# Performance work log

Measured on AMD Instinct MI355X. Metric: run time of the kernel, lower is better.

## Reference

```python
import jax, jax.numpy as jnp
import numpy as np

N_NODES = 10000
N_EDGES = 160000
BATCH = 16
F_IN = 32          # NODE_EMBED_SIZE
HEADS = 4
HDIM = 4
HC = HEADS * HDIM  # 16
N_LAYERS = 4
OBS_DIM = 100
NUM_OUT = 30
HID = 128
POOL_OUT = 15


def setup_inputs() -> dict:
    key = jax.random.key(0)
    ks = jax.random.split(key, 26)
    s = 0.1
    d = {}
    d["x"] = jax.random.normal(ks[0], (BATCH, N_NODES, F_IN), jnp.float32)
    d["obs"] = jax.random.normal(ks[1], (BATCH, OBS_DIM), jnp.float32)
    d["src"] = jax.random.randint(ks[2], (N_EDGES,), 0, N_NODES)
    d["dst"] = jax.random.randint(ks[3], (N_EDGES,), 0, N_NODES)
    # layer 0 (in=F_IN), layers 1..3 (in=HC) GATv2 params
    d["W0l"] = jax.random.normal(ks[4], (F_IN, HC)) * s
    d["W0r"] = jax.random.normal(ks[5], (F_IN, HC)) * s
    d["b0l"] = jnp.zeros((HC,), jnp.float32)
    d["b0r"] = jnp.zeros((HC,), jnp.float32)
    d["Wl"] = jax.random.normal(ks[6], (N_LAYERS - 1, HC, HC)) * s
    d["Wr"] = jax.random.normal(ks[7], (N_LAYERS - 1, HC, HC)) * s
    d["bl"] = jnp.zeros((N_LAYERS - 1, HC), jnp.float32)
    d["br"] = jnp.zeros((N_LAYERS - 1, HC), jnp.float32)
    d["att"] = jax.random.normal(ks[8], (N_LAYERS, HEADS, HDIM)) * s
    d["bias"] = jnp.zeros((N_LAYERS, HC), jnp.float32)
    # mean-pool aggregator projection to 15
    d["Wp"] = jax.random.normal(ks[9], (HC, POOL_OUT)) * s
    d["bp"] = jnp.zeros((POOL_OUT,), jnp.float32)
    # hybrid policy head: cat([feat15, obs100]) -> 128 -> 128 -> num_outputs
    d["W1"] = jax.random.normal(ks[10], (POOL_OUT + OBS_DIM, HID)) * s
    d["b1"] = jnp.zeros((HID,), jnp.float32)
    d["W2"] = jax.random.normal(ks[11], (HID, HID)) * s
    d["b2"] = jnp.zeros((HID,), jnp.float32)
    d["W3"] = jax.random.normal(ks[12], (HID, NUM_OUT)) * s
    d["b3"] = jnp.zeros((NUM_OUT,), jnp.float32)
    return d


def _gatv2_layer(x, src, dst, Wl, Wr, bl, br, att, bias):
    # x: [B,N,F]; src/dst: [E'] (self loops included); att: [H,C]
    B, N, _ = x.shape
    H, C = att.shape
    xl = (x @ Wl + bl).reshape(B, N, H, C)  # source transform
    xr = (x @ Wr + br).reshape(B, N, H, C)  # target transform
    z = jax.nn.leaky_relu(xl[:, src] + xr[:, dst], negative_slope=0.2)  # [B,E,H,C]
    e = jnp.einsum('behc,hc->ebh', z, att)  # [E,B,H] edge-major for segment ops
    m = jax.lax.stop_gradient(jax.ops.segment_max(e, dst, num_segments=N))
    m = jnp.where(jnp.isfinite(m), m, 0.0)
    ex = jnp.exp(e - m[dst])
    ssum = jax.ops.segment_sum(ex, dst, num_segments=N)
    alpha = ex / (ssum[dst] + 1e-16)  # softmax over incoming edges of dst
    msg = xl[:, src] * jnp.transpose(alpha, (1, 0, 2))[..., None]  # [B,E,H,C]
    out = jax.ops.segment_sum(jnp.transpose(msg, (1, 0, 2, 3)), dst, num_segments=N)
    return jnp.transpose(out, (1, 0, 2, 3)).reshape(B, N, H * C) + bias


def reference(x, obs, src, dst, W0l, W0r, b0l, b0r, Wl, Wr, bl, br, att, bias,
              Wp, bp, W1, b1, W2, b2, W3, b3):
    N = x.shape[1]
    loop = jnp.arange(N, dtype=src.dtype)  # PyG add_self_loops=True
    src_f = jnp.concatenate([src, loop])
    dst_f = jnp.concatenate([dst, loop])
    h = _gatv2_layer(x, src_f, dst_f, W0l, W0r, b0l, b0r, att[0], bias[0])
    for l in range(N_LAYERS - 1):
        h = _gatv2_layer(h, src_f, dst_f, Wl[l], Wr[l], bl[l], br[l], att[l + 1], bias[l + 1])
    feat = h.mean(axis=1) @ Wp + bp  # mean-pool aggregator -> [B,15]
    z1 = jnp.tanh(jnp.concatenate([feat, obs], axis=1) @ W1 + b1)
    z2 = jnp.tanh(z1 @ W2 + b2)
    return z2 @ W3 + b3  # logits [B, NUM_OUT]
```

## Files before the change

kernel.cpp:

```cpp
#include <hip/hip_runtime.h>
#include <cstdint>
#include <cstddef>

#define NN   10000
#define NE   160000
#define NB   16
#define FIN  32
#define HC   16
#define NH   4
#define HD   4
#define OBSD 100
#define NOUT 30
#define HIDD 128
#define PO   15
#define BCAP 64
#define NBUCKET 64
#define EG   2500
#define HSM  8884

typedef float floatx2 __attribute__((ext_vector_type(2)));

__device__ inline uint32_t pack_fp8x4(float a, float b, float c, float d) {
    int p = __builtin_amdgcn_cvt_pk_fp8_f32(a, b, 0, false);
    p = __builtin_amdgcn_cvt_pk_fp8_f32(c, d, p, true);
    return (uint32_t)p;
}

__device__ inline float4 shfl_xor4(float4 v, int m) {
    float4 r;
    r.x = __shfl_xor(v.x, m, 64);
    r.y = __shfl_xor(v.y, m, 64);
    r.z = __shfl_xor(v.z, m, 64);
    r.w = __shfl_xor(v.w, m, 64);
    return r;
}

__global__ void k_build_xform0(const int* __restrict__ src, const int* __restrict__ dst,
                               int* __restrict__ cnt, int* __restrict__ bucket,
                               const float* __restrict__ x,
                               const float* __restrict__ Wlg, const float* __restrict__ Wrg,
                               const float* __restrict__ blg, const float* __restrict__ brg,
                               uint32_t* __restrict__ xl, uint32_t* __restrict__ xr) {
    int bid = blockIdx.x;
    if (bid < 625) {
        int e = bid * 256 + threadIdx.x;
        if (e < NE) {
            int d = dst[e];
            int p = atomicAdd(&cnt[d], 1);
            if (p < BCAP) bucket[(size_t)d * BCAP + p] = src[e];
        }
        return;
    }
    __shared__ float sWl[FIN * HC], sWr[FIN * HC], sbl[HC], sbr[HC];
    for (int i = threadIdx.x; i < FIN * HC; i += 256) { sWl[i] = Wlg[i]; sWr[i] = Wrg[i]; }
    if (threadIdx.x < HC) { sbl[threadIdx.x] = blg[threadIdx.x]; sbr[threadIdx.x] = brg[threadIdx.x]; }
    __syncthreads();
    int local = bid - 625;
    int b = local / 40;
    int n = (local % 40) * 256 + threadIdx.x;
    if (n >= NN) return;
    const float* xp = x + ((size_t)b * NN + n) * FIN;
    float row[FIN];
#pragma unroll
    for (int f = 0; f < FIN; f++) row[f] = xp[f];
    float al[HC], ar[HC];
#pragma unroll
    for (int c = 0; c < HC; c++) { al[c] = sbl[c]; ar[c] = sbr[c]; }
#pragma unroll
    for (int f = 0; f < FIN; f++) {
        float v = row[f];
#pragma unroll
        for (int c = 0; c < HC; c++) {
            al[c] = fmaf(v, sWl[f * HC + c], al[c]);
            ar[c] = fmaf(v, sWr[f * HC + c], ar[c]);
        }
    }
    uint32_t* xlo = xl + ((size_t)n * NB + b) * 4;
    uint32_t* xro = xr + ((size_t)n * NB + b) * 4;
#pragma unroll
    for (int hh = 0; hh < 4; hh++) {
        xlo[hh] = pack_fp8x4(al[hh * 4 + 0], al[hh * 4 + 1], al[hh * 4 + 2], al[hh * 4 + 3]);
        xro[hh] = pack_fp8x4(ar[hh * 4 + 0], ar[hh * 4 + 1], ar[hh * 4 + 2], ar[hh * 4 + 3]);
    }
}

template <int MODE>
__global__ __launch_bounds__(256, 4)
void k_edge_f(const uint32_t* __restrict__ xl, const uint32_t* __restrict__ xr,
              const int* __restrict__ cntg, const int* __restrict__ bucket,
              const float* __restrict__ attg, const float* __restrict__ biasg,
              const float* __restrict__ Wln, const float* __restrict__ Wrn,
              const float* __restrict__ bln, const float* __restrict__ brn,
              uint32_t* __restrict__ xl_o, uint32_t* __restrict__ xr_o,
              float* __restrict__ pool_part, int* __restrict__ done_sub,
              int* __restrict__ master,
              const float* __restrict__ obs,
              const float* __restrict__ Wp, const float* __restrict__ bp,
              const float* __restrict__ W1, const float* __restrict__ b1,
              const float* __restrict__ W2, const float* __restrict__ b2,
              const float* __restrict__ W3, const float* __restrict__ b3,
              float* __restrict__ out) {
    __shared__ float smem[MODE == 2 ? HSM : 1024];
    const int tid = threadIdx.x;

    if (MODE == 2 && blockIdx.x >= EG) {
        const int b = blockIdx.x - EG;
        float* stage = smem;
        float* sPart = smem + 8192;
        float* sPool = smem + 8256;
        float* sIn   = smem + 8272;
        float* s1a   = smem + 8388;
        float* s2a   = smem + 8516;
        float* sWp   = smem + 8644;
        for (int i = tid; i < 2048; i += 256)
            ((float4*)stage)[i] = ((const float4*)W1)[i];
        if (tid < HC * PO) sWp[tid] = Wp[tid];
        for (int k = tid; k < OBSD; k += 256) sIn[PO + k] = obs[b * OBSD + k];
        if (tid == 0) {
            while (__hip_atomic_load(master, __ATOMIC_RELAXED,
                                     __HIP_MEMORY_SCOPE_AGENT) < NBUCKET) {
                __builtin_amdgcn_s_sleep(16);
            }
        }
        __syncthreads();
        if (tid < 64) {
            int c = tid & 15, q4 = tid >> 4;
            float ps = 0.f;
#pragma unroll
            for (int q = q4; q < NBUCKET; q += 4)
                ps += __hip_atomic_load(&pool_part[q * 256 + b * HC + c],
                                        __ATOMIC_RELAXED, __HIP_MEMORY_SCOPE_AGENT);
            sPart[tid] = ps;
        }
        __syncthreads();
        if (tid < HC)
            sPool[tid] = (sPart[tid] + sPart[16 + tid] + sPart[32 + tid] + sPart[48 + tid]) * (1.0f / NN);
        __syncthreads();
        if (tid < PO) {
            float acc = bp[tid];
#pragma unroll
            for (int c = 0; c < HC; c++) acc = fmaf(sPool[c], sWp[c * PO + tid], acc);
            sIn[tid] = acc;
        }
        __syncthreads();
        float acc1 = (tid < HIDD) ? b1[tid] : 0.f;
        if (tid < HIDD)
            for (int k = 0; k < 64; k++) acc1 = fmaf(sIn[k], stage[k * HIDD + tid], acc1);
        __syncthreads();
        {
            for (int i = tid; i < 1632; i += 256)
                ((float4*)stage)[i] = ((const float4*)(W1 + 64 * HIDD))[i];
            __syncthreads();
            if (tid < HIDD) {
                for (int k = 0; k < 51; k++) acc1 = fmaf(sIn[64 + k], stage[k * HIDD + tid], acc1);
                s1a[tid] = tanhf(acc1);
            }
            __syncthreads();
        }
        float acc2 = (tid < HIDD) ? b2[tid] : 0.f;
#pragma unroll
        for (int ch = 0; ch < 2; ch++) {
            for (int i = tid; i < 2048; i += 256)
                ((float4*)stage)[i] = ((const float4*)(W2 + ch * 64 * HIDD))[i];
            __syncthreads();
            if (tid < HIDD)
                for (int k = 0; k < 64; k++) acc2 = fmaf(s1a[ch * 64 + k], stage[k * HIDD + tid], acc2);
            __syncthreads();
        }
        if (tid < HIDD) s2a[tid] = tanhf(acc2);
        for (int i = tid; i < 960; i += 256)
            ((float4*)stage)[i] = ((const float4*)W3)[i];
        __syncthreads();
        if (tid < NOUT) {
            float acc3 = b3[tid];
            for (int k = 0; k < HIDD; k++) acc3 = fmaf(s2a[k], stage[k * NOUT + tid], acc3);
            out[b * NOUT + tid] = acc3;
        }
        return;
    }

    if (MODE == 1) {
        smem[tid] = Wln[tid];
        smem[256 + tid] = Wrn[tid];
        if (tid < HC) { smem[512 + tid] = bln[tid]; smem[528 + tid] = brn[tid]; }
        __syncthreads();
    }
    const int wave = (blockIdx.x * 256 + tid) >> 6;
    const int lane = tid & 63;
    const int n = wave;
    const int h = lane & 3;
    const float4 a4 = *(const float4*)(attg + h * HD);
    const float4 bias4 = *(const float4*)(biasg + h * HD);
    float4 xr4;
    {
        uint32_t xrr = xr[(size_t)n * 64 + lane];
        floatx2 q0 = __builtin_amdgcn_cvt_pk_f32_fp8((int)xrr, false);
        floatx2 q1 = __builtin_amdgcn_cvt_pk_f32_fp8((int)xrr, true);
        xr4 = make_float4(q0.x, q0.y, q1.x, q1.y);
    }
    int vidx = bucket[(size_t)n * BCAP + lane];
    int cnt = __builtin_amdgcn_readfirstlane(cntg[n]);
    cnt = cnt < BCAP ? cnt : BCAP;
    float4 acc = make_float4(0.f, 0.f, 0.f, 0.f);
    float ssum = 0.f;

#define EDGE_CORE(RAW, EXPR)                                                  \
    {                                                                         \
        floatx2 f0 = __builtin_amdgcn_cvt_pk_f32_fp8((int)(RAW), false);      \
        floatx2 f1 = __builtin_amdgcn_cvt_pk_f32_fp8((int)(RAW), true);       \
        float z0 = f0.x + xr4.x; z0 = fmaxf(z0, 0.2f * z0);                   \
        float z1 = f0.y + xr4.y; z1 = fmaxf(z1, 0.2f * z1);                   \
        float z2 = f1.x + xr4.z; z2 = fmaxf(z2, 0.2f * z2);                   \
        float z3 = f1.y + xr4.w; z3 = fmaxf(z3, 0.2f * z3);                   \
        float e = fmaf(z3, a4.w, fmaf(z2, a4.z, fmaf(z1, a4.y, z0 * a4.x)));  \
        float ex = EXPR;                                                      \
        ssum += ex;                                                           \
        acc.x = fmaf(ex, f0.x, acc.x);                                        \
        acc.y = fmaf(ex, f0.y, acc.y);                                        \
        acc.z = fmaf(ex, f1.x, acc.z);                                        \
        acc.w = fmaf(ex, f1.y, acc.w);                                        \
    }
#define EDGE_BODY1(RAW)    EDGE_CORE(RAW, __expf(e))
#define EDGE_BODYM(RAW, M) EDGE_CORE(RAW, (M) * __expf(e))
#define GATHER(S) xl[(size_t)(S) * 64 + lane]

    { const uint32_t r = GATHER(n); EDGE_BODY1(r); }
    if (cnt > 0) {
        int i = 0;
        for (; i + 16 <= cnt; i += 16) {
            uint32_t r[16];
#pragma unroll
            for (int u = 0; u < 16; u++) {
                int s = __builtin_amdgcn_readlane(vidx, i + u);
                r[u] = GATHER(s);
            }
#pragma unroll
            for (int u = 0; u < 16; u++) EDGE_BODY1(r[u]);
        }
        int rem = cnt - i;
        if (rem > 8) {
            uint32_t r[16];
#pragma unroll
            for (int u = 0; u < 16; u++) {
                int e2 = i + u;
                int ec = e2 < cnt ? e2 : cnt - 1;
                int s = __builtin_amdgcn_readlane(vidx, ec);
                r[u] = GATHER(s);
            }
#pragma unroll
            for (int u = 0; u < 16; u++) {
                float m = (i + u < cnt) ? 1.0f : 0.0f;
                EDGE_BODYM(r[u], m);
            }
        } else if (rem > 0) {
            uint32_t r[8];
#pragma unroll
            for (int u = 0; u < 8; u++) {
                int e2 = i + u;
                int ec = e2 < cnt ? e2 : cnt - 1;
                int s = __builtin_amdgcn_readlane(vidx, ec);
                r[u] = GATHER(s);
            }
#pragma unroll
            for (int u = 0; u < 8; u++) {
                float m = (i + u < cnt) ? 1.0f : 0.0f;
                EDGE_BODYM(r[u], m);
            }
        }
    }
#undef GATHER
#undef EDGE_BODY1
#undef EDGE_BODYM
#undef EDGE_CORE

    float inv = 1.0f / (ssum + 1e-16f);
    float4 o;
    o.x = fmaf(acc.x, inv, bias4.x);
    o.y = fmaf(acc.y, inv, bias4.y);
    o.z = fmaf(acc.z, inv, bias4.z);
    o.w = fmaf(acc.w, inv, bias4.w);

    if (MODE == 1) {
        float accl[4], accr[4];
#pragma unroll
        for (int cj = 0; cj < 4; cj++) {
            accl[cj] = smem[512 + h * 4 + cj];
            accr[cj] = smem[528 + h * 4 + cj];
        }
#pragma unroll
        for (int m = 0; m < 4; m++) {
            float4 vals = (m == 0) ? o : shfl_xor4(o, m);
            int fbase = ((h ^ m) << 2);
            float vv[4] = {vals.x, vals.y, vals.z, vals.w};
#pragma unroll
            for (int j = 0; j < 4; j++) {
                const float4 wl = *(const float4*)&smem[(fbase + j) * HC + (h << 2)];
                const float4 wr = *(const float4*)&smem[256 + (fbase + j) * HC + (h << 2)];
                float v = vv[j];
                accl[0] = fmaf(v, wl.x, accl[0]);
                accl[1] = fmaf(v, wl.y, accl[1]);
                accl[2] = fmaf(v, wl.z, accl[2]);
                accl[3] = fmaf(v, wl.w, accl[3]);
                accr[0] = fmaf(v, wr.x, accr[0]);
                accr[1] = fmaf(v, wr.y, accr[1]);
                accr[2] = fmaf(v, wr.z, accr[2]);
                accr[3] = fmaf(v, wr.w, accr[3]);
            }
        }
        xl_o[(size_t)n * 64 + lane] = pack_fp8x4(accl[0], accl[1], accl[2], accl[3]);
        xr_o[(size_t)n * 64 + lane] = pack_fp8x4(accr[0], accr[1], accr[2], accr[3]);
    } else {
        *(float4*)&smem[tid * 4] = o;
        __syncthreads();
        if (tid < 64) {
            float4 s0 = *(const float4*)&smem[tid * 4];
            float4 s1v = *(const float4*)&smem[(64 + tid) * 4];
            float4 s2v = *(const float4*)&smem[(128 + tid) * 4];
            float4 s3v = *(const float4*)&smem[(192 + tid) * 4];
            float* dp = pool_part + (blockIdx.x & (NBUCKET - 1)) * 256 + tid * 4;
            atomicAdd(dp + 0, s0.x + s1v.x + s2v.x + s3v.x);
            atomicAdd(dp + 1, s0.y + s1v.y + s2v.y + s3v.y);
            atomicAdd(dp + 2, s0.z + s1v.z + s2v.z + s3v.z);
            atomicAdd(dp + 3, s0.w + s1v.w + s2v.w + s3v.w);
        }
        if (tid == 0) {
            asm volatile("s_waitcnt vmcnt(0)" ::: "memory");
            int s = blockIdx.x & 63;
            int quota = (s < (EG & 63)) ? (EG / 64 + 1) : (EG / 64);
            int old = __hip_atomic_fetch_add(&done_sub[s], 1, __ATOMIC_RELAXED,
                                             __HIP_MEMORY_SCOPE_AGENT);
            if (old == quota - 1)
                __hip_atomic_fetch_add(master, 1, __ATOMIC_RELAXED,
                                       __HIP_MEMORY_SCOPE_AGENT);
        }
    }
}

extern "C" void kernel_launch(void* const* d_in, const int* in_sizes, int n_in,
                              void* d_out, int out_size, void* d_ws, size_t ws_size,
                              hipStream_t stream) {
    const float* x    = (const float*)d_in[0];
    const float* obs  = (const float*)d_in[1];
    const int*   src  = (const int*)d_in[2];
    const int*   dst  = (const int*)d_in[3];
    const float* W0l  = (const float*)d_in[4];
    const float* W0r  = (const float*)d_in[5];
    const float* b0l  = (const float*)d_in[6];
    const float* b0r  = (const float*)d_in[7];
    const float* Wl   = (const float*)d_in[8];
    const float* Wr   = (const float*)d_in[9];
    const float* bl   = (const float*)d_in[10];
    const float* br   = (const float*)d_in[11];
    const float* att  = (const float*)d_in[12];
    const float* bias = (const float*)d_in[13];
    const float* Wp   = (const float*)d_in[14];
    const float* bp   = (const float*)d_in[15];
    const float* W1   = (const float*)d_in[16];
    const float* b1   = (const float*)d_in[17];
    const float* W2   = (const float*)d_in[18];
    const float* b2   = (const float*)d_in[19];
    const float* W3   = (const float*)d_in[20];
    const float* b3   = (const float*)d_in[21];
    float* out = (float*)d_out;

    size_t off = 0;
    auto take = [&](size_t bytes) -> void* {
        void* ptr = (char*)d_ws + off;
        off += (bytes + 255) & ~(size_t)255;
        return ptr;
    };
    int*      cnt       = (int*)take(NN * sizeof(int));
    float*    pool_part = (float*)take(NBUCKET * 256 * sizeof(float));
    int*      done_sub  = (int*)take(64 * sizeof(int));
    int*      master    = (int*)take(64 * sizeof(int));
    int*      bucket    = (int*)take((size_t)NN * BCAP * sizeof(int));
    uint32_t* xlA       = (uint32_t*)take((size_t)NN * 64 * sizeof(uint32_t));
    uint32_t* xrA       = (uint32_t*)take((size_t)NN * 64 * sizeof(uint32_t));
    uint32_t* xlB       = (uint32_t*)take((size_t)NN * 64 * sizeof(uint32_t));
    uint32_t* xrB       = (uint32_t*)take((size_t)NN * 64 * sizeof(uint32_t));

    size_t zspan = (size_t)((char*)(master + 64) - (char*)cnt);
    hipMemsetAsync(cnt, 0, zspan, stream);

    k_build_xform0<<<625 + 40 * NB, 256, 0, stream>>>(src, dst, cnt, bucket,
                                                      x, W0l, W0r, b0l, b0r, xlA, xrA);

    k_edge_f<1><<<EG, 256, 0, stream>>>(xlA, xrA, cnt, bucket,
                                        att + 0 * 16, bias + 0 * 16,
                                        Wl + 0 * 256, Wr + 0 * 256, bl + 0 * 16, br + 0 * 16,
                                        xlB, xrB, nullptr, nullptr, nullptr,
                                        nullptr, nullptr, nullptr, nullptr, nullptr,
                                        nullptr, nullptr, nullptr, nullptr, nullptr);
    k_edge_f<1><<<EG, 256, 0, stream>>>(xlB, xrB, cnt, bucket,
                                        att + 1 * 16, bias + 1 * 16,
                                        Wl + 1 * 256, Wr + 1 * 256, bl + 1 * 16, br + 1 * 16,
                                        xlA, xrA, nullptr, nullptr, nullptr,
                                        nullptr, nullptr, nullptr, nullptr, nullptr,
                                        nullptr, nullptr, nullptr, nullptr, nullptr);
    k_edge_f<1><<<EG, 256, 0, stream>>>(xlA, xrA, cnt, bucket,
                                        att + 2 * 16, bias + 2 * 16,
                                        Wl + 2 * 256, Wr + 2 * 256, bl + 2 * 16, br + 2 * 16,
                                        xlB, xrB, nullptr, nullptr, nullptr,
                                        nullptr, nullptr, nullptr, nullptr, nullptr,
                                        nullptr, nullptr, nullptr, nullptr, nullptr);
    k_edge_f<2><<<EG + NB, 256, 0, stream>>>(xlB, xrB, cnt, bucket,
                                             att + 3 * 16, bias + 3 * 16,
                                             nullptr, nullptr, nullptr, nullptr,
                                             nullptr, nullptr, pool_part, done_sub,
                                             master, obs, Wp, bp, W1, b1, W2, b2,
                                             W3, b3, out);
}
```

Measured before the change: 125.7 us.

## Switch edge kernels to persistent grid-stride waves and vectorize input row loads

```diff
diff --git a/kernel.cpp b/kernel.cpp
--- a/kernel.cpp
+++ b/kernel.cpp
@@ -15,7 +15,8 @@
 #define PO   15
 #define BCAP 64
 #define NBUCKET 64
-#define EG   2500
+#define EGB  640
+#define NWAVES (EGB * 4)
 #define HSM  8884
 
 typedef float floatx2 __attribute__((ext_vector_type(2)));
@@ -59,10 +60,11 @@
     int b = local / 40;
     int n = (local % 40) * 256 + threadIdx.x;
     if (n >= NN) return;
-    const float* xp = x + ((size_t)b * NN + n) * FIN;
-    float row[FIN];
-#pragma unroll
-    for (int f = 0; f < FIN; f++) row[f] = xp[f];
+    const float4* xp4 = (const float4*)(x + ((size_t)b * NN + n) * FIN);
+    float4 rowv[8];
+#pragma unroll
+    for (int f4 = 0; f4 < 8; f4++) rowv[f4] = xp4[f4];
+    const float* row = (const float*)rowv;
     float al[HC], ar[HC];
 #pragma unroll
     for (int c = 0; c < HC; c++) { al[c] = sbl[c]; ar[c] = sbr[c]; }
@@ -103,8 +105,8 @@
     __shared__ float smem[MODE == 2 ? HSM : 1024];
     const int tid = threadIdx.x;
 
-    if (MODE == 2 && blockIdx.x >= EG) {
-        const int b = blockIdx.x - EG;
+    if (MODE == 2 && blockIdx.x >= EGB) {
+        const int b = blockIdx.x - EGB;
         float* stage = smem;
         float* sPart = smem + 8192;
         float* sPool = smem + 8256;
@@ -185,24 +187,26 @@
         if (tid < HC) { smem[512 + tid] = bln[tid]; smem[528 + tid] = brn[tid]; }
         __syncthreads();
     }
-    const int wave = (blockIdx.x * 256 + tid) >> 6;
+    const int wv   = blockIdx.x * 4 + (tid >> 6);
     const int lane = tid & 63;
-    const int n = wave;
-    const int h = lane & 3;
+    const int h    = lane & 3;
     const float4 a4 = *(const float4*)(attg + h * HD);
     const float4 bias4 = *(const float4*)(biasg + h * HD);
-    float4 xr4;
-    {
-        uint32_t xrr = xr[(size_t)n * 64 + lane];
-        floatx2 q0 = __builtin_amdgcn_cvt_pk_f32_fp8((int)xrr, false);
-        floatx2 q1 = __builtin_amdgcn_cvt_pk_f32_fp8((int)xrr, true);
-        xr4 = make_float4(q0.x, q0.y, q1.x, q1.y);
-    }
-    int vidx = bucket[(size_t)n * BCAP + lane];
-    int cnt = __builtin_amdgcn_readfirstlane(cntg[n]);
-    cnt = cnt < BCAP ? cnt : BCAP;
-    float4 acc = make_float4(0.f, 0.f, 0.f, 0.f);
-    float ssum = 0.f;
+    float psum0 = 0.f, psum1 = 0.f, psum2 = 0.f, psum3 = 0.f;
+
+    for (int n = wv; n < NN; n += NWAVES) {
+        float4 xr4;
+        {
+            uint32_t xrr = xr[(size_t)n * 64 + lane];
+            floatx2 q0 = __builtin_amdgcn_cvt_pk_f32_fp8((int)xrr, false);
+            floatx2 q1 = __builtin_amdgcn_cvt_pk_f32_fp8((int)xrr, true);
+            xr4 = make_float4(q0.x, q0.y, q1.x, q1.y);
+        }
+        int vidx = bucket[(size_t)n * BCAP + lane];
+        int cnt = __builtin_amdgcn_readfirstlane(cntg[n]);
+        cnt = cnt < BCAP ? cnt : BCAP;
+        float4 acc = make_float4(0.f, 0.f, 0.f, 0.f);
+        float ssum = 0.f;
 
 #define EDGE_CORE(RAW, EXPR)                                                  \
     {                                                                         \
@@ -224,93 +228,98 @@
 #define EDGE_BODYM(RAW, M) EDGE_CORE(RAW, (M) * __expf(e))
 #define GATHER(S) xl[(size_t)(S) * 64 + lane]
 
-    { const uint32_t r = GATHER(n); EDGE_BODY1(r); }
-    if (cnt > 0) {
-        int i = 0;
-        for (; i + 16 <= cnt; i += 16) {
-            uint32_t r[16];
-#pragma unroll
-            for (int u = 0; u < 16; u++) {
-                int s = __builtin_amdgcn_readlane(vidx, i + u);
-                r[u] = GATHER(s);
-            }
-#pragma unroll
-            for (int u = 0; u < 16; u++) EDGE_BODY1(r[u]);
-        }
-        int rem = cnt - i;
-        if (rem > 8) {
-            uint32_t r[16];
-#pragma unroll
-            for (int u = 0; u < 16; u++) {
-                int e2 = i + u;
-                int ec = e2 < cnt ? e2 : cnt - 1;
-                int s = __builtin_amdgcn_readlane(vidx, ec);
-                r[u] = GATHER(s);
-            }
-#pragma unroll
-            for (int u = 0; u < 16; u++) {
-                float m = (i + u < cnt) ? 1.0f : 0.0f;
-                EDGE_BODYM(r[u], m);
-            }
-        } else if (rem > 0) {
-            uint32_t r[8];
-#pragma unroll
-            for (int u = 0; u < 8; u++) {
-                int e2 = i + u;
-                int ec = e2 < cnt ? e2 : cnt - 1;
-                int s = __builtin_amdgcn_readlane(vidx, ec);
-                r[u] = GATHER(s);
-            }
-#pragma unroll
-            for (int u = 0; u < 8; u++) {
-                float m = (i + u < cnt) ? 1.0f : 0.0f;
-                EDGE_BODYM(r[u], m);
-            }
-        }
-    }
+        { const uint32_t r = GATHER(n); EDGE_BODY1(r); }
+        if (cnt > 0) {
+            int i = 0;
+            for (; i + 16 <= cnt; i += 16) {
+                uint32_t r[16];
+#pragma unroll
+                for (int u = 0; u < 16; u++) {
+                    int s = __builtin_amdgcn_readlane(vidx, i + u);
+                    r[u] = GATHER(s);
+                }
+#pragma unroll
+                for (int u = 0; u < 16; u++) EDGE_BODY1(r[u]);
+            }
+            int rem = cnt - i;
+            if (rem > 8) {
+                uint32_t r[16];
+#pragma unroll
+                for (int u = 0; u < 16; u++) {
+                    int e2 = i + u;
+                    int ec = e2 < cnt ? e2 : cnt - 1;
+                    int s = __builtin_amdgcn_readlane(vidx, ec);
+                    r[u] = GATHER(s);
+                }
+#pragma unroll
+                for (int u = 0; u < 16; u++) {
+                    float m = (i + u < cnt) ? 1.0f : 0.0f;
+                    EDGE_BODYM(r[u], m);
+                }
+            } else if (rem > 0) {
+                uint32_t r[8];
+#pragma unroll
+                for (int u = 0; u < 8; u++) {
+                    int e2 = i + u;
+                    int ec = e2 < cnt ? e2 : cnt - 1;
+                    int s = __builtin_amdgcn_readlane(vidx, ec);
+                    r[u] = GATHER(s);
+                }
+#pragma unroll
+                for (int u = 0; u < 8; u++) {
+                    float m = (i + u < cnt) ? 1.0f : 0.0f;
+                    EDGE_BODYM(r[u], m);
+                }
+            }
+        }
 #undef GATHER
 #undef EDGE_BODY1
 #undef EDGE_BODYM
 #undef EDGE_CORE
 
-    float inv = 1.0f / (ssum + 1e-16f);
-    float4 o;
-    o.x = fmaf(acc.x, inv, bias4.x);
-    o.y = fmaf(acc.y, inv, bias4.y);
-    o.z = fmaf(acc.z, inv, bias4.z);
-    o.w = fmaf(acc.w, inv, bias4.w);
-
-    if (MODE == 1) {
-        float accl[4], accr[4];
-#pragma unroll
-        for (int cj = 0; cj < 4; cj++) {
-            accl[cj] = smem[512 + h * 4 + cj];
-            accr[cj] = smem[528 + h * 4 + cj];
-        }
-#pragma unroll
-        for (int m = 0; m < 4; m++) {
-            float4 vals = (m == 0) ? o : shfl_xor4(o, m);
-            int fbase = ((h ^ m) << 2);
-            float vv[4] = {vals.x, vals.y, vals.z, vals.w};
-#pragma unroll
-            for (int j = 0; j < 4; j++) {
-                const float4 wl = *(const float4*)&smem[(fbase + j) * HC + (h << 2)];
-                const float4 wr = *(const float4*)&smem[256 + (fbase + j) * HC + (h << 2)];
-                float v = vv[j];
-                accl[0] = fmaf(v, wl.x, accl[0]);
-                accl[1] = fmaf(v, wl.y, accl[1]);
-                accl[2] = fmaf(v, wl.z, accl[2]);
-                accl[3] = fmaf(v, wl.w, accl[3]);
-                accr[0] = fmaf(v, wr.x, accr[0]);
-                accr[1] = fmaf(v, wr.y, accr[1]);
-                accr[2] = fmaf(v, wr.z, accr[2]);
-                accr[3] = fmaf(v, wr.w, accr[3]);
-            }
-        }
-        xl_o[(size_t)n * 64 + lane] = pack_fp8x4(accl[0], accl[1], accl[2], accl[3]);
-        xr_o[(size_t)n * 64 + lane] = pack_fp8x4(accr[0], accr[1], accr[2], accr[3]);
-    } else {
-        *(float4*)&smem[tid * 4] = o;
+        float inv = 1.0f / (ssum + 1e-16f);
+        float4 o;
+        o.x = fmaf(acc.x, inv, bias4.x);
+        o.y = fmaf(acc.y, inv, bias4.y);
+        o.z = fmaf(acc.z, inv, bias4.z);
+        o.w = fmaf(acc.w, inv, bias4.w);
+
+        if (MODE == 1) {
+            float accl[4], accr[4];
+#pragma unroll
+            for (int cj = 0; cj < 4; cj++) {
+                accl[cj] = smem[512 + h * 4 + cj];
+                accr[cj] = smem[528 + h * 4 + cj];
+            }
+#pragma unroll
+            for (int m = 0; m < 4; m++) {
+                float4 vals = (m == 0) ? o : shfl_xor4(o, m);
+                int fbase = ((h ^ m) << 2);
+                float vv[4] = {vals.x, vals.y, vals.z, vals.w};
+#pragma unroll
+                for (int j = 0; j < 4; j++) {
+                    const float4 wl = *(const float4*)&smem[(fbase + j) * HC + (h << 2)];
+                    const float4 wr = *(const float4*)&smem[256 + (fbase + j) * HC + (h << 2)];
+                    float v = vv[j];
+                    accl[0] = fmaf(v, wl.x, accl[0]);
+                    accl[1] = fmaf(v, wl.y, accl[1]);
+                    accl[2] = fmaf(v, wl.z, accl[2]);
+                    accl[3] = fmaf(v, wl.w, accl[3]);
+                    accr[0] = fmaf(v, wr.x, accr[0]);
+                    accr[1] = fmaf(v, wr.y, accr[1]);
+                    accr[2] = fmaf(v, wr.z, accr[2]);
+                    accr[3] = fmaf(v, wr.w, accr[3]);
+                }
+            }
+            xl_o[(size_t)n * 64 + lane] = pack_fp8x4(accl[0], accl[1], accl[2], accl[3]);
+            xr_o[(size_t)n * 64 + lane] = pack_fp8x4(accr[0], accr[1], accr[2], accr[3]);
+        } else {
+            psum0 += o.x; psum1 += o.y; psum2 += o.z; psum3 += o.w;
+        }
+    }
+
+    if (MODE == 2) {
+        *(float4*)&smem[tid * 4] = make_float4(psum0, psum1, psum2, psum3);
         __syncthreads();
         if (tid < 64) {
             float4 s0 = *(const float4*)&smem[tid * 4];
@@ -326,7 +335,7 @@
         if (tid == 0) {
             asm volatile("s_waitcnt vmcnt(0)" ::: "memory");
             int s = blockIdx.x & 63;
-            int quota = (s < (EG & 63)) ? (EG / 64 + 1) : (EG / 64);
+            const int quota = EGB / 64;
             int old = __hip_atomic_fetch_add(&done_sub[s], 1, __ATOMIC_RELAXED,
                                              __HIP_MEMORY_SCOPE_AGENT);
             if (old == quota - 1)
@@ -385,28 +394,28 @@
     k_build_xform0<<<625 + 40 * NB, 256, 0, stream>>>(src, dst, cnt, bucket,
                                                       x, W0l, W0r, b0l, b0r, xlA, xrA);
 
-    k_edge_f<1><<<EG, 256, 0, stream>>>(xlA, xrA, cnt, bucket,
-                                        att + 0 * 16, bias + 0 * 16,
-                                        Wl + 0 * 256, Wr + 0 * 256, bl + 0 * 16, br + 0 * 16,
-                                        xlB, xrB, nullptr, nullptr, nullptr,
-                                        nullptr, nullptr, nullptr, nullptr, nullptr,
-                                        nullptr, nullptr, nullptr, nullptr, nullptr);
-    k_edge_f<1><<<EG, 256, 0, stream>>>(xlB, xrB, cnt, bucket,
-                                        att + 1 * 16, bias + 1 * 16,
-                                        Wl + 1 * 256, Wr + 1 * 256, bl + 1 * 16, br + 1 * 16,
-                                        xlA, xrA, nullptr, nullptr, nullptr,
-                                        nullptr, nullptr, nullptr, nullptr, nullptr,
-                                        nullptr, nullptr, nullptr, nullptr, nullptr);
-    k_edge_f<1><<<EG, 256, 0, stream>>>(xlA, xrA, cnt, bucket,
-                                        att + 2 * 16, bias + 2 * 16,
-                                        Wl + 2 * 256, Wr + 2 * 256, bl + 2 * 16, br + 2 * 16,
-                                        xlB, xrB, nullptr, nullptr, nullptr,
-                                        nullptr, nullptr, nullptr, nullptr, nullptr,
-                                        nullptr, nullptr, nullptr, nullptr, nullptr);
-    k_edge_f<2><<<EG + NB, 256, 0, stream>>>(xlB, xrB, cnt, bucket,
-                                             att + 3 * 16, bias + 3 * 16,
-                                             nullptr, nullptr, nullptr, nullptr,
-                                             nullptr, nullptr, pool_part, done_sub,
-                                             master, obs, Wp, bp, W1, b1, W2, b2,
-                                             W3, b3, out);
+    k_edge_f<1><<<EGB, 256, 0, stream>>>(xlA, xrA, cnt, bucket,
+                                         att + 0 * 16, bias + 0 * 16,
+                                         Wl + 0 * 256, Wr + 0 * 256, bl + 0 * 16, br + 0 * 16,
+                                         xlB, xrB, nullptr, nullptr, nullptr,
+                                         nullptr, nullptr, nullptr, nullptr, nullptr,
+                                         nullptr, nullptr, nullptr, nullptr, nullptr);
+    k_edge_f<1><<<EGB, 256, 0, stream>>>(xlB, xrB, cnt, bucket,
+                                         att + 1 * 16, bias + 1 * 16,
+                                         Wl + 1 * 256, Wr + 1 * 256, bl + 1 * 16, br + 1 * 16,
+                                         xlA, xrA, nullptr, nullptr, nullptr,
+                                         nullptr, nullptr, nullptr, nullptr, nullptr,
+                                         nullptr, nullptr, nullptr, nullptr, nullptr);
+    k_edge_f<1><<<EGB, 256, 0, stream>>>(xlA, xrA, cnt, bucket,
+                                         att + 2 * 16, bias + 2 * 16,
+                                         Wl + 2 * 256, Wr + 2 * 256, bl + 2 * 16, br + 2 * 16,
+                                         xlB, xrB, nullptr, nullptr, nullptr,
+                                         nullptr, nullptr, nullptr, nullptr, nullptr,
+                                         nullptr, nullptr, nullptr, nullptr, nullptr);
+    k_edge_f<2><<<EGB + NB, 256, 0, stream>>>(xlB, xrB, cnt, bucket,
+                                              att + 3 * 16, bias + 3 * 16,
+                                              nullptr, nullptr, nullptr, nullptr,
+                                              nullptr, nullptr, pool_part, done_sub,
+                                              master, obs, Wp, bp, W1, b1, W2, b2,
+                                              W3, b3, out);
 }
```

New measurement: 233.4 us. 1.86x slower.
